# Optimization experiments

Hardware: AMD Instinct MI355X
Metric: run time of the kernel (lower is better)

Reference implementation:

```python
import jax, jax.numpy as jnp
import numpy as np
import math

B, SQ, SK, D = 32, 2048, 2048, 128


def setup_inputs() -> dict:
    key = jax.random.key(0)
    kq, kk, kv = jax.random.split(key, 3)
    queries = jax.random.normal(kq, (B, SQ, D), dtype=jnp.float32)
    keys = jax.random.normal(kk, (B, SK, D), dtype=jnp.float32)
    values = jax.random.normal(kv, (B, SK, D), dtype=jnp.float32)
    # causal mask: True = masked (future positions), broadcast over batch
    causal = jnp.triu(jnp.ones((SQ, SK), dtype=bool), k=1)
    mask = jnp.broadcast_to(causal, (B, SQ, SK))
    return {"queries": queries, "keys": keys, "values": values, "mask": mask}


def reference(queries, keys, values, mask):
    d = queries.shape[-1]
    scale = 1.0 / math.sqrt(d)
    # [B, Sq, Sk] score matrix (the module materializes this explicitly)
    scores = jnp.einsum("bqd,bkd->bqk", queries, keys) * scale
    scores = jnp.where(mask, -jnp.inf, scores)
    attn = jax.nn.softmax(scores, axis=-1)
    # dropout p=0.0 -> identity (eval parity)
    return jnp.einsum("bqk,bkd->bqd", attn, values)
```

## Files before the change

### kernel.cpp

```cpp
#include <hip/hip_runtime.h>
#include <hip/hip_bf16.h>

#define NB   32
#define SQL  2048
#define DH   128
#define QBLK 128
#define KBLK 64
#define NKT  (SQL / KBLK)
#define TILEB 16384

typedef __attribute__((ext_vector_type(4)))  float f32x4;
typedef __attribute__((ext_vector_type(16))) float f32x16;
typedef __attribute__((ext_vector_type(8)))  short s16x8;
typedef __attribute__((ext_vector_type(4)))  unsigned int u32x4;

__device__ __forceinline__ unsigned int cvtpk_bf16(float lo, float hi) {
  unsigned int r;
  asm("v_cvt_pk_bf16_f32 %0, %1, %2" : "=v"(r) : "v"(lo), "v"(hi));
  return r;
}
#define PLSWAP(x, y) asm volatile("v_permlane32_swap_b32 %0, %1" : "+v"(x), "+v"(y))

__device__ __forceinline__ unsigned int pk2(float lo, float hi) {
  unsigned short a = __builtin_bit_cast(unsigned short, __float2bfloat16(lo));
  unsigned short b = __builtin_bit_cast(unsigned short, __float2bfloat16(hi));
  return (unsigned int)a | ((unsigned int)b << 16);
}

#define AS1(p) ((const __attribute__((address_space(1))) void*)(p))
#define AS3(p) ((__attribute__((address_space(3))) void*)(p))

__global__ __launch_bounds__(256)
void prep_kv(const float* __restrict__ Kg, const float* __restrict__ Vg,
             char* __restrict__ wsK, char* __restrict__ wsV) {
  const int blk = blockIdx.x;
  const int b   = blk >> 5;
  const int kt  = blk & 31;
  const int tid = threadIdx.x;
  const float* Ksrc = Kg + ((size_t)b * SQL + (size_t)kt * KBLK) * DH;
  const float* Vsrc = Vg + ((size_t)b * SQL + (size_t)kt * KBLK) * DH;
  char* Kdst = wsK + (size_t)blk * TILEB;
  char* Vdst = wsV + (size_t)blk * TILEB;

  {
    const int q16 = tid & 15;
    const int r0  = tid >> 4;
    #pragma unroll
    for (int it = 0; it < 4; ++it) {
      const int r = r0 + 16 * it;
      const float* src = Ksrc + (size_t)r * DH + 8 * q16;
      f32x4 a = *(const f32x4*)(src);
      f32x4 d = *(const f32x4*)(src + 4);
      u32x4 w;
      w[0] = pk2(a[0], a[1]); w[1] = pk2(a[2], a[3]);
      w[2] = pk2(d[0], d[1]); w[3] = pk2(d[2], d[3]);
      *(u32x4*)(Kdst + ((r * 256 + 16 * q16) ^ ((r & 7) << 4))) = w;
    }
  }
  {
    const int kq = tid & 15;
    const int dq = tid >> 4;
    #pragma unroll
    for (int it = 0; it < 2; ++it) {
      const int d0 = 4 * dq + 64 * it;
      f32x4 rv[4];
      #pragma unroll
      for (int j = 0; j < 4; ++j)
        rv[j] = *(const f32x4*)(Vsrc + (size_t)(4 * kq + j) * DH + d0);
      #pragma unroll
      for (int j2 = 0; j2 < 4; ++j2) {
        const int dd = d0 + j2;
        uint2 w = make_uint2(pk2(rv[0][j2], rv[1][j2]), pk2(rv[2][j2], rv[3][j2]));
        *(uint2*)(Vdst + ((dd * 128 + 8 * kq) ^ ((dd & 7) << 4))) = w;
      }
    }
  }
}

__global__ __launch_bounds__(256, 2)
void attn_fwd(const float* __restrict__ Qg, const char* __restrict__ wsK,
              const char* __restrict__ wsV, float* __restrict__ Og) {
  __shared__ __align__(16) char smem[65536];

  const int tid  = threadIdx.x;
  const int wid  = tid >> 6;
  const int lane = tid & 63;
  const int hi   = lane >> 5;
  const int c    = lane & 31;

  const int i   = blockIdx.x;
  const int p   = i & 1;
  const int q3  = (i >> 1) & 7;
  const int b   = (i >> 4) & 31;
  const int qtb = (b & 16) ? (15 - q3) : q3;
  const int qt  = p ? qtb : (15 - qtb);
  const int qb  = qt * QBLK;
  const int nt  = 2 * qt + 2;

  const float* Qb = Qg + (size_t)b * SQL * DH;
  float* Ob = Og + (size_t)b * SQL * DH;
  const char* Ktiles = wsK + (size_t)b * NKT * TILEB;
  const char* Vtiles = wsV + (size_t)b * NKT * TILEB;

  const float qscale = 0.08838834764831845f * 1.4426950408889634f;

  s16x8 qf[8];
  {
    const float* qr = Qb + (size_t)(qb + 32*wid + c) * DH + 8*hi;
    #pragma unroll
    for (int ds = 0; ds < 8; ++ds) {
      f32x4 a = *(const f32x4*)(qr + 16*ds);
      f32x4 d = *(const f32x4*)(qr + 16*ds + 4);
      u32x4 w;
      w[0] = pk2(a[0]*qscale, a[1]*qscale);
      w[1] = pk2(a[2]*qscale, a[3]*qscale);
      w[2] = pk2(d[0]*qscale, d[1]*qscale);
      w[3] = pk2(d[2]*qscale, d[3]*qscale);
      qf[ds] = __builtin_bit_cast(s16x8, w);
    }
  }

  f32x16 oacc[4];
  #pragma unroll
  for (int nb = 0; nb < 4; ++nb) oacc[nb] = (f32x16){0.f};
  float m_run = -1e30f, l_run = 0.f;

  const int qglob = qb + 32*wid + c;
  const int qhiw  = qb + 32*wid + 31;
  const int qlow  = qb + 32*wid;

  auto STAGE = [&](int t) {
    const char* ks = Ktiles + (size_t)t * TILEB + tid * 16;
    const char* vs = Vtiles + (size_t)t * TILEB + tid * 16;
    char* kl = smem + (t & 1) * 16384 + wid * 1024;
    char* vl = smem + 32768 + (t & 1) * 16384 + wid * 1024;
    #pragma unroll
    for (int j = 0; j < 4; ++j) {
      __builtin_amdgcn_global_load_lds(AS1(ks + j * 4096), AS3(kl + j * 4096), 16, 0, 0);
      __builtin_amdgcn_global_load_lds(AS1(vs + j * 4096), AS3(vl + j * 4096), 16, 0, 0);
    }
  };

  STAGE(0);
  STAGE(1);

  for (int t = 0; t < nt; ++t) {
    if (t == nt - 1) asm volatile("s_waitcnt vmcnt(0)" ::: "memory");
    else             asm volatile("s_waitcnt vmcnt(8)" ::: "memory");
    __builtin_amdgcn_s_barrier();
    __builtin_amdgcn_sched_barrier(0);

    const int kb = t * KBLK;
    const char* Kl = smem + (t & 1) * 16384;
    const char* Vl = smem + 32768 + (t & 1) * 16384;

    if (kb <= qhiw) {
      f32x16 sacc[2];
      sacc[0] = (f32x16){0.f};
      sacc[1] = (f32x16){0.f};
      __builtin_amdgcn_s_setprio(1);
      #pragma unroll
      for (int ds = 0; ds < 8; ++ds) {
        #pragma unroll
        for (int mb = 0; mb < 2; ++mb) {
          const int row = 32*mb + c;
          s16x8 kf = *(const s16x8*)(Kl + ((row*256 + 32*ds + 16*hi) ^ ((c & 7) << 4)));
          sacc[mb] = __builtin_amdgcn_mfma_f32_32x32x16_bf16(kf, qf[ds], sacc[mb], 0, 0, 0);
        }
      }
      __builtin_amdgcn_s_setprio(0);

      if (kb + KBLK - 1 > qlow) {
        #pragma unroll
        for (int mb = 0; mb < 2; ++mb)
          #pragma unroll
          for (int r = 0; r < 16; ++r) {
            const int kk = kb + 32*mb + (r & 3) + 8*(r >> 2) + 4*hi;
            if (kk > qglob) sacc[mb][r] = -1e30f;
          }
      }

      float mx[8];
      #pragma unroll
      for (int e = 0; e < 8; ++e)
        mx[e] = fmaxf(fmaxf(sacc[0][e], sacc[0][e+8]), fmaxf(sacc[1][e], sacc[1][e+8]));
      mx[0] = fmaxf(mx[0], mx[4]); mx[1] = fmaxf(mx[1], mx[5]);
      mx[2] = fmaxf(mx[2], mx[6]); mx[3] = fmaxf(mx[3], mx[7]);
      float tmax = fmaxf(fmaxf(mx[0], mx[1]), fmaxf(mx[2], mx[3]));
      tmax = fmaxf(tmax, __shfl_xor(tmax, 32));

      if (!__all(tmax <= m_run + 8.0f)) {
        const float mnew  = fmaxf(m_run, tmax);
        const float alpha = exp2f(m_run - mnew);
        #pragma unroll
        for (int r = 0; r < 16; ++r) {
          float av = __shfl(alpha, (r & 3) + 8*(r >> 2) + 4*hi);
          #pragma unroll
          for (int nb = 0; nb < 4; ++nb) oacc[nb][r] *= av;
        }
        l_run *= alpha;
        m_run = mnew;
      }

      float lsum = 0.f;
      unsigned int u0[8], u1[8];
      {
        float pz[16];
        #pragma unroll
        for (int r = 0; r < 16; ++r) pz[r] = exp2f(sacc[0][r] - m_run);
        lsum += ((pz[0]+pz[1])+(pz[2]+pz[3])) + ((pz[4]+pz[5])+(pz[6]+pz[7]))
              + ((pz[8]+pz[9])+(pz[10]+pz[11])) + ((pz[12]+pz[13])+(pz[14]+pz[15]));
        #pragma unroll
        for (int w = 0; w < 8; ++w) u0[w] = cvtpk_bf16(pz[2*w], pz[2*w+1]);
      }
      {
        float pz[16];
        #pragma unroll
        for (int r = 0; r < 16; ++r) pz[r] = exp2f(sacc[1][r] - m_run);
        lsum += ((pz[0]+pz[1])+(pz[2]+pz[3])) + ((pz[4]+pz[5])+(pz[6]+pz[7]))
              + ((pz[8]+pz[9])+(pz[10]+pz[11])) + ((pz[12]+pz[13])+(pz[14]+pz[15]));
        #pragma unroll
        for (int w = 0; w < 8; ++w) u1[w] = cvtpk_bf16(pz[2*w], pz[2*w+1]);
      }
      lsum += __shfl_xor(lsum, 32);
      l_run += lsum;

      PLSWAP(u0[0], u0[2]); PLSWAP(u0[1], u0[3]);
      PLSWAP(u0[4], u0[6]); PLSWAP(u0[5], u0[7]);
      PLSWAP(u1[0], u1[2]); PLSWAP(u1[1], u1[3]);
      PLSWAP(u1[4], u1[6]); PLSWAP(u1[5], u1[7]);
      s16x8 pa[4];
      { u32x4 w = {u0[0], u0[1], u0[2], u0[3]}; pa[0] = __builtin_bit_cast(s16x8, w); }
      { u32x4 w = {u0[4], u0[5], u0[6], u0[7]}; pa[1] = __builtin_bit_cast(s16x8, w); }
      { u32x4 w = {u1[0], u1[1], u1[2], u1[3]}; pa[2] = __builtin_bit_cast(s16x8, w); }
      { u32x4 w = {u1[4], u1[5], u1[6], u1[7]}; pa[3] = __builtin_bit_cast(s16x8, w); }

      __builtin_amdgcn_s_setprio(1);
      #pragma unroll
      for (int nb = 0; nb < 4; ++nb) {
        #pragma unroll
        for (int ks = 0; ks < 4; ++ks) {
          const int row = 32*nb + c;
          s16x8 vf = *(const s16x8*)(Vl + ((row*128 + 32*ks + 16*hi) ^ ((c & 7) << 4)));
          oacc[nb] = __builtin_amdgcn_mfma_f32_32x32x16_bf16(pa[ks], vf, oacc[nb], 0, 0, 0);
        }
      }
      __builtin_amdgcn_s_setprio(0);
    }

    __builtin_amdgcn_s_barrier();
    if (t + 2 < nt) STAGE(t + 2);
  }

  const float linv = 1.0f / l_run;
  float* Orow = Ob + (size_t)(qb + 32*wid) * DH;
  #pragma unroll
  for (int r = 0; r < 16; ++r) {
    const int q = (r & 3) + 8*(r >> 2) + 4*hi;
    float lv = __shfl(linv, q);
    #pragma unroll
    for (int nb = 0; nb < 4; ++nb)
      Orow[(size_t)q * DH + 32*nb + c] = oacc[nb][r] * lv;
  }
}

extern "C" void kernel_launch(void* const* d_in, const int* in_sizes, int n_in,
                              void* d_out, int out_size, void* d_ws, size_t ws_size,
                              hipStream_t stream) {
  const float* Q = (const float*)d_in[0];
  const float* K = (const float*)d_in[1];
  const float* V = (const float*)d_in[2];
  float* O = (float*)d_out;
  char* wsK = (char*)d_ws;
  char* wsV = (char*)d_ws + (size_t)NB * NKT * TILEB;

  prep_kv<<<dim3(NB * NKT), dim3(256), 0, stream>>>(K, V, wsK, wsV);
  attn_fwd<<<dim3(NB * (SQL / QBLK)), dim3(256), 0, stream>>>(Q, wsK, wsV, O);
}
```

Before: 89.42 us.

## Single-buffer V tile to fit three blocks per CU with split K/V pipeline

Cuts LDS from 64KB to 48KB by giving V a single buffer instead of a double buffer, so launch bounds can target three blocks per CU. K and V staging are split: V for the next tile is issued right after the PV MFMAs, with an extra wait and barrier before PV. The block-to-work mapping is also reordered into two halves that pair causal-heavy and light tiles. The cost is an extra barrier per iteration, less prefetch lead time for V, and tighter register pressure at higher occupancy.

```diff
diff --git a/kernel.cpp b/kernel.cpp
--- a/kernel.cpp
+++ b/kernel.cpp
@@ -77,10 +77,10 @@
   }
 }
 
-__global__ __launch_bounds__(256, 2)
+__global__ __launch_bounds__(256, 3)
 void attn_fwd(const float* __restrict__ Qg, const char* __restrict__ wsK,
               const char* __restrict__ wsV, float* __restrict__ Og) {
-  __shared__ __align__(16) char smem[65536];
+  __shared__ __align__(16) char smem[49152];
 
   const int tid  = threadIdx.x;
   const int wid  = tid >> 6;
@@ -88,14 +88,13 @@
   const int hi   = lane >> 5;
   const int c    = lane & 31;
 
-  const int i   = blockIdx.x;
-  const int p   = i & 1;
-  const int q3  = (i >> 1) & 7;
-  const int b   = (i >> 4) & 31;
-  const int qtb = (b & 16) ? (15 - q3) : q3;
-  const int qt  = p ? qtb : (15 - qtb);
-  const int qb  = qt * QBLK;
-  const int nt  = 2 * qt + 2;
+  const int i    = blockIdx.x;
+  const int half = i >> 8;
+  const int j    = i & 255;
+  const int qt   = half ? (15 - (j >> 5)) : (j >> 5);
+  const int b    = j & 31;
+  const int qb   = qt * QBLK;
+  const int nt   = 2 * qt + 2;
 
   const float* Qb = Qg + (size_t)b * SQL * DH;
   float* Ob = Og + (size_t)b * SQL * DH;
@@ -129,32 +128,39 @@
   const int qhiw  = qb + 32*wid + 31;
   const int qlow  = qb + 32*wid;
 
-  auto STAGE = [&](int t) {
+  auto STAGE_K = [&](int t) {
     const char* ks = Ktiles + (size_t)t * TILEB + tid * 16;
+    char* kl = smem + (t & 1) * 16384 + wid * 1024;
+    #pragma unroll
+    for (int jj = 0; jj < 4; ++jj)
+      __builtin_amdgcn_global_load_lds(AS1(ks + jj * 4096), AS3(kl + jj * 4096), 16, 0, 0);
+  };
+  auto STAGE_V = [&](int t) {
     const char* vs = Vtiles + (size_t)t * TILEB + tid * 16;
-    char* kl = smem + (t & 1) * 16384 + wid * 1024;
-    char* vl = smem + 32768 + (t & 1) * 16384 + wid * 1024;
-    #pragma unroll
-    for (int j = 0; j < 4; ++j) {
-      __builtin_amdgcn_global_load_lds(AS1(ks + j * 4096), AS3(kl + j * 4096), 16, 0, 0);
-      __builtin_amdgcn_global_load_lds(AS1(vs + j * 4096), AS3(vl + j * 4096), 16, 0, 0);
-    }
+    char* vl = smem + 32768 + wid * 1024;
+    #pragma unroll
+    for (int jj = 0; jj < 4; ++jj)
+      __builtin_amdgcn_global_load_lds(AS1(vs + jj * 4096), AS3(vl + jj * 4096), 16, 0, 0);
   };
 
-  STAGE(0);
-  STAGE(1);
+  STAGE_K(0);
+  STAGE_V(0);
+  STAGE_K(1);
+
+  const char* Vl = smem + 32768;
 
   for (int t = 0; t < nt; ++t) {
-    if (t == nt - 1) asm volatile("s_waitcnt vmcnt(0)" ::: "memory");
+    if (t == nt - 1) asm volatile("s_waitcnt vmcnt(4)" ::: "memory");
     else             asm volatile("s_waitcnt vmcnt(8)" ::: "memory");
     __builtin_amdgcn_s_barrier();
     __builtin_amdgcn_sched_barrier(0);
 
     const int kb = t * KBLK;
     const char* Kl = smem + (t & 1) * 16384;
-    const char* Vl = smem + 32768 + (t & 1) * 16384;
-
-    if (kb <= qhiw) {
+    const bool active = (kb <= qhiw);
+
+    s16x8 pa[4];
+    if (active) {
       f32x16 sacc[2];
       sacc[0] = (f32x16){0.f};
       sacc[1] = (f32x16){0.f};
@@ -202,26 +208,23 @@
         m_run = mnew;
       }
 
-      float lsum = 0.f;
+      float lsa = 0.f, lsb = 0.f;
       unsigned int u0[8], u1[8];
-      {
-        float pz[16];
-        #pragma unroll
-        for (int r = 0; r < 16; ++r) pz[r] = exp2f(sacc[0][r] - m_run);
-        lsum += ((pz[0]+pz[1])+(pz[2]+pz[3])) + ((pz[4]+pz[5])+(pz[6]+pz[7]))
-              + ((pz[8]+pz[9])+(pz[10]+pz[11])) + ((pz[12]+pz[13])+(pz[14]+pz[15]));
-        #pragma unroll
-        for (int w = 0; w < 8; ++w) u0[w] = cvtpk_bf16(pz[2*w], pz[2*w+1]);
-      }
-      {
-        float pz[16];
-        #pragma unroll
-        for (int r = 0; r < 16; ++r) pz[r] = exp2f(sacc[1][r] - m_run);
-        lsum += ((pz[0]+pz[1])+(pz[2]+pz[3])) + ((pz[4]+pz[5])+(pz[6]+pz[7]))
-              + ((pz[8]+pz[9])+(pz[10]+pz[11])) + ((pz[12]+pz[13])+(pz[14]+pz[15]));
-        #pragma unroll
-        for (int w = 0; w < 8; ++w) u1[w] = cvtpk_bf16(pz[2*w], pz[2*w+1]);
-      }
+      #pragma unroll
+      for (int w = 0; w < 8; ++w) {
+        float p0 = exp2f(sacc[0][2*w]     - m_run);
+        float p1 = exp2f(sacc[0][2*w + 1] - m_run);
+        lsa += p0 + p1;
+        u0[w] = cvtpk_bf16(p0, p1);
+      }
+      #pragma unroll
+      for (int w = 0; w < 8; ++w) {
+        float p0 = exp2f(sacc[1][2*w]     - m_run);
+        float p1 = exp2f(sacc[1][2*w + 1] - m_run);
+        lsb += p0 + p1;
+        u1[w] = cvtpk_bf16(p0, p1);
+      }
+      float lsum = lsa + lsb;
       lsum += __shfl_xor(lsum, 32);
       l_run += lsum;
 
@@ -229,12 +232,18 @@
       PLSWAP(u0[4], u0[6]); PLSWAP(u0[5], u0[7]);
       PLSWAP(u1[0], u1[2]); PLSWAP(u1[1], u1[3]);
       PLSWAP(u1[4], u1[6]); PLSWAP(u1[5], u1[7]);
-      s16x8 pa[4];
       { u32x4 w = {u0[0], u0[1], u0[2], u0[3]}; pa[0] = __builtin_bit_cast(s16x8, w); }
       { u32x4 w = {u0[4], u0[5], u0[6], u0[7]}; pa[1] = __builtin_bit_cast(s16x8, w); }
       { u32x4 w = {u1[0], u1[1], u1[2], u1[3]}; pa[2] = __builtin_bit_cast(s16x8, w); }
       { u32x4 w = {u1[4], u1[5], u1[6], u1[7]}; pa[3] = __builtin_bit_cast(s16x8, w); }
-
+    }
+
+    if (t == nt - 1) asm volatile("s_waitcnt vmcnt(0)" ::: "memory");
+    else             asm volatile("s_waitcnt vmcnt(4)" ::: "memory");
+    __builtin_amdgcn_s_barrier();
+    __builtin_amdgcn_sched_barrier(0);
+
+    if (active) {
       __builtin_amdgcn_s_setprio(1);
       #pragma unroll
       for (int nb = 0; nb < 4; ++nb) {
@@ -249,7 +258,8 @@
     }
 
     __builtin_amdgcn_s_barrier();
-    if (t + 2 < nt) STAGE(t + 2);
+    if (t + 1 < nt) STAGE_V(t + 1);
+    if (t + 2 < nt) STAGE_K(t + 2);
   }
 
   const float linv = 1.0f / l_run;
```

New measurement: 193.1 us. +115.9%, slower.
